# Kernel tuning notes

Measured on AMD Instinct MI355X. Metric: run time of the kernel, lower is better.

The kernel has to match this reference:

```python
import jax, jax.numpy as jnp
import numpy as np

N = 50000      # nodes
E = 800000     # edges
DIN = 500      # input feature dim
H = 128        # hidden dim
C = 40         # num classes
B = 10000      # batch_size (labeled nodes)
L = 9          # n_layers
K = 5          # topk neighbors
ALPHA = 0.5
THETA = 1.0
ETA = 0.5


def setup_inputs() -> dict:
    key = jax.random.key(0)
    ks = jax.random.split(key, 10)
    x = jax.random.normal(ks[0], (N, DIN), jnp.float32)
    edge_index = jax.random.randint(ks[1], (2, E), 0, N, dtype=jnp.int32)
    edge_weight = jax.random.uniform(ks[2], (E,), jnp.float32)
    y = jax.random.randint(ks[3], (B,), 0, C, dtype=jnp.int32)
    W1 = jax.random.normal(ks[4], (DIN, H), jnp.float32) * 0.05
    b1 = jnp.zeros((H,), jnp.float32)
    conv_w1 = jax.random.normal(ks[5], (L, H, H), jnp.float32) * 0.05
    conv_w2 = jax.random.normal(ks[6], (L, H, H), jnp.float32) * 0.05
    W2 = jax.random.normal(ks[7], (H, C), jnp.float32) * 0.05
    b2 = jnp.zeros((C,), jnp.float32)
    return dict(x=x, edge_index=edge_index, edge_weight=edge_weight, y=y,
                batch_size=B, W1=W1, b1=b1, conv_w1=conv_w1, conv_w2=conv_w2,
                W2=W2, b2=b2)


def _spmm(edge_index, edge_weight, h):
    # out[row] += w * h[col]  (sparse adj_t @ h)
    row, col = edge_index[0], edge_index[1]
    msg = h[col] * edge_weight[:, None]           # [E, H]
    return jax.ops.segment_sum(msg, row, num_segments=N)


def reference(x, edge_index, edge_weight, y, batch_size, W1, b1, conv_w1, conv_w2, W2, b2):
    # eval mode: dropout is identity, no diagonal mask in label fusion
    h = jax.nn.relu(x @ W1 + b1)                  # [N, H]
    x0 = h
    for l in range(L):
        beta = float(np.log(THETA / (l + 1) + 1.0))
        p = _spmm(edge_index, edge_weight, h) * (1.0 - ALPHA)   # propagated, scaled
        xr = ALPHA * x0                                          # initial residual
        out = ((1.0 - beta) * p + beta * (p @ conv_w1[l])
               + (1.0 - beta) * xr + beta * (xr @ conv_w2[l]))
        h = jax.nn.relu(h + out)
    emb = h[:batch_size]                          # [B, H]
    logits = h @ W2 + b2
    p_lc = jax.nn.log_softmax(logits[:batch_size], axis=1)       # [B, C]
    # kNN label fusion: cosine similarity, topk, exp-weighted one-hot sum
    an = emb / jnp.clip(jnp.linalg.norm(emb, axis=1, keepdims=True), 1e-8)
    sim = an @ an.T                               # [B, B]
    vals, idx = jax.lax.top_k(sim, K)             # [B, K]
    w = jnp.exp(jax.lax.stop_gradient(vals))      # topk computed under no_grad
    onehot = jax.nn.one_hot(y, C, dtype=jnp.float32)             # [B, C]
    fused = jnp.einsum('bk,bkc->bc', w, onehot[idx])             # [B, C]
    p_sim = jax.nn.log_softmax(fused, axis=1)
    final = ETA * p_lc + (1.0 - ETA) * p_sim
    return final, emb
```

## Files before the change

kernel.cpp:

```cpp
#include <hip/hip_runtime.h>
#include <hip/hip_bf16.h>
#include <math.h>

#define Nn  50000
#define NR  50048
#define En  800000
#define DIN 500
#define Hd  128
#define Cc  40
#define Bb  10000
#define Ll  9
#define KT  5

typedef short bf16x8 __attribute__((ext_vector_type(8)));
typedef unsigned short u16x8 __attribute__((ext_vector_type(8)));
typedef float f32x4 __attribute__((ext_vector_type(4)));

__device__ inline float bf2f(unsigned short u) {
  union { unsigned int i; float f; } c; c.i = (unsigned int)u << 16; return c.f;
}
__device__ inline unsigned short f2bf(float f) {
  __hip_bfloat16 b = __float2bfloat16(f);
  return *(unsigned short*)&b;
}

__global__ __launch_bounds__(256) void k_pack_w1(const float* __restrict__ W1,
                                                 unsigned short* __restrict__ W1p) {
  const int id = blockIdx.x * 256 + threadIdx.x;
  if (id >= 65536) return;
  const int j = id & 7, col = (id >> 3) & 127, qk = id >> 10;
  const int k = (qk >> 2) * 32 + (qk & 3) * 8 + j;
  W1p[id] = f2bf((k < DIN) ? W1[(size_t)k * Hd + col] : 0.f);
}

__global__ __launch_bounds__(256) void k_pack_wc(const float* __restrict__ cw1,
    const float* __restrict__ cw2, unsigned short* __restrict__ Wcp) {
  const int id = blockIdx.x * 256 + threadIdx.x;
  if (id >= 294912) return;
  const int j = id & 7, col = (id >> 3) & 127, qk = (id >> 10) & 31, l = id >> 15;
  const int k = (qk >> 2) * 32 + (qk & 3) * 8 + j;
  float v;
  if (k < 128) v = cw1[((size_t)l * 128 + k) * 128 + col];
  else         v = 0.5f * cw2[((size_t)l * 128 + (k - 128)) * 128 + col];
  Wcp[id] = f2bf(v);
}

__global__ __launch_bounds__(256) void k_in(const float* __restrict__ x,
    const unsigned short* __restrict__ W1p, const float* __restrict__ b1,
    unsigned short* __restrict__ hb, unsigned short* __restrict__ x0b) {
  const int tid = threadIdx.x;
  const int wv = tid >> 6, lane = tid & 63;
  const int lrow = lane & 15, quad = lane >> 4;
  const int row0 = blockIdx.x * 64;
  const int ar = row0 + wv * 16 + lrow;
  f32x4 acc[8];
#pragma unroll
  for (int t = 0; t < 8; ++t) acc[t] = (f32x4){0.f, 0.f, 0.f, 0.f};

  for (int kk = 0; kk < 16; ++kk) {
    const int kbase = kk * 32 + quad * 8;
    float av[8];
    if (ar < Nn) {
      if (kk < 15) {
        const float4 p0 = *(const float4*)(x + (size_t)ar * DIN + kbase);
        const float4 p1 = *(const float4*)(x + (size_t)ar * DIN + kbase + 4);
        av[0] = p0.x; av[1] = p0.y; av[2] = p0.z; av[3] = p0.w;
        av[4] = p1.x; av[5] = p1.y; av[6] = p1.z; av[7] = p1.w;
      } else {
#pragma unroll
        for (int j = 0; j < 8; ++j)
          av[j] = (kbase + j < DIN) ? x[(size_t)ar * DIN + kbase + j] : 0.f;
      }
    } else {
#pragma unroll
      for (int j = 0; j < 8; ++j) av[j] = 0.f;
    }
    bf16x8 af;
#pragma unroll
    for (int j = 0; j < 8; ++j) af[j] = (short)f2bf(av[j]);
#pragma unroll
    for (int nt = 0; nt < 8; ++nt) {
      const bf16x8 bf = *(const bf16x8*)(W1p + ((size_t)(kk * 4 + quad) * 128 + nt * 16 + lrow) * 8);
      acc[nt] = __builtin_amdgcn_mfma_f32_16x16x32_bf16(af, bf, acc[nt], 0, 0, 0);
    }
  }

  __shared__ float sacc[64 * 132];
#pragma unroll
  for (int nt = 0; nt < 8; ++nt)
#pragma unroll
    for (int i = 0; i < 4; ++i)
      sacc[(wv * 16 + quad * 4 + i) * 132 + nt * 16 + lrow] = acc[nt][i];
  __syncthreads();

  const int row = tid >> 2, cs = (tid & 3) * 32;
  const int gr = row0 + row;
  if (gr < Nn) {
#pragma unroll
    for (int g = 0; g < 4; ++g) {
      const int c0 = cs + g * 8;
      float v[8];
#pragma unroll
      for (int j = 0; j < 8; ++j)
        v[j] = fmaxf(sacc[row * 132 + c0 + j] + b1[c0 + j], 0.f);
      u16x8 ob;
#pragma unroll
      for (int j = 0; j < 8; ++j) ob[j] = f2bf(v[j]);
      *(u16x8*)(hb + (size_t)gr * Hd + c0) = ob;
      *(u16x8*)(x0b + (size_t)gr * Hd + c0) = ob;
    }
  }
}

__global__ void k_hist(const int* __restrict__ rows, int* __restrict__ counts) {
  int e = blockIdx.x * 256 + threadIdx.x;
  if (e < En) atomicAdd(&counts[rows[e]], 1);
}

__global__ __launch_bounds__(256) void k_scan2(const int* __restrict__ counts,
                                               int* __restrict__ rptr) {
  __shared__ int sdata[256];
  const int b = blockIdx.x, tid = threadIdx.x;
  const int npre = b << 8;
  int s0 = 0, s1 = 0, s2 = 0, s3 = 0;
  int i = tid;
  for (; i + 768 < npre; i += 1024) {
    s0 += counts[i]; s1 += counts[i + 256]; s2 += counts[i + 512]; s3 += counts[i + 768];
  }
  for (; i < npre; i += 256) s0 += counts[i];
  sdata[tid] = s0 + s1 + s2 + s3;
  __syncthreads();
  for (int off = 128; off > 0; off >>= 1) {
    if (tid < off) sdata[tid] += sdata[tid + off];
    __syncthreads();
  }
  const int base = sdata[0];
  __syncthreads();
  const int gi = npre + tid;
  int v = (gi < Nn) ? counts[gi] : 0;
  sdata[tid] = v;
  __syncthreads();
  for (int off = 1; off < 256; off <<= 1) {
    int t = (tid >= off) ? sdata[tid - off] : 0;
    __syncthreads();
    sdata[tid] += t;
    __syncthreads();
  }
  if (gi < Nn) rptr[gi + 1] = base + sdata[tid];
  if (b == 0 && tid == 0) rptr[0] = 0;
}

__global__ void k_scatter(const int* __restrict__ rows, const int* __restrict__ cols,
                          const float* __restrict__ w, const int* __restrict__ ptr,
                          int* __restrict__ fill, int* __restrict__ csr_col,
                          float* __restrict__ csr_w) {
  int e = blockIdx.x * 256 + threadIdx.x;
  if (e >= En) return;
  int r = rows[e];
  int pos = atomicAdd(&fill[r], 1);
  int d = ptr[r] + pos;
  csr_col[d] = cols[e];
  csr_w[d] = w[e];
}

__global__ __launch_bounds__(256) void k_spmm(const int* __restrict__ ptr,
    const int* __restrict__ csr_col, const float* __restrict__ csr_w,
    const unsigned short* __restrict__ hb, unsigned short* __restrict__ pb) {
  const int wave = (blockIdx.x * 256 + threadIdx.x) >> 6;
  const int lane = threadIdx.x & 63;
  const int g = lane >> 4;
  const int fl = lane & 15;
  if (wave >= Nn) return;
  const int s = ptr[wave], e_end = ptr[wave + 1];
  float acc[8];
#pragma unroll
  for (int j = 0; j < 8; ++j) acc[j] = 0.f;

  auto acc8 = [&](uint4 v, float w) {
    union { unsigned int i; float f; } t;
    t.i = v.x << 16;         acc[0] += w * t.f;
    t.i = v.x & 0xFFFF0000u; acc[1] += w * t.f;
    t.i = v.y << 16;         acc[2] += w * t.f;
    t.i = v.y & 0xFFFF0000u; acc[3] += w * t.f;
    t.i = v.z << 16;         acc[4] += w * t.f;
    t.i = v.z & 0xFFFF0000u; acc[5] += w * t.f;
    t.i = v.w << 16;         acc[6] += w * t.f;
    t.i = v.w & 0xFFFF0000u; acc[7] += w * t.f;
  };

  int e = s + g;
  for (; e + 12 < e_end; e += 16) {
    const int c0 = csr_col[e];
    const int c1 = csr_col[e + 4];
    const int c2 = csr_col[e + 8];
    const int c3 = csr_col[e + 12];
    const float w0 = csr_w[e];
    const float w1 = csr_w[e + 4];
    const float w2 = csr_w[e + 8];
    const float w3 = csr_w[e + 12];
    const uint4 v0 = *(const uint4*)(hb + (size_t)c0 * Hd + fl * 8);
    const uint4 v1 = *(const uint4*)(hb + (size_t)c1 * Hd + fl * 8);
    const uint4 v2 = *(const uint4*)(hb + (size_t)c2 * Hd + fl * 8);
    const uint4 v3 = *(const uint4*)(hb + (size_t)c3 * Hd + fl * 8);
    acc8(v0, w0); acc8(v1, w1); acc8(v2, w2); acc8(v3, w3);
  }
  for (; e + 4 < e_end; e += 8) {
    const int c0 = csr_col[e];
    const int c1 = csr_col[e + 4];
    const float w0 = csr_w[e];
    const float w1 = csr_w[e + 4];
    const uint4 v0 = *(const uint4*)(hb + (size_t)c0 * Hd + fl * 8);
    const uint4 v1 = *(const uint4*)(hb + (size_t)c1 * Hd + fl * 8);
    acc8(v0, w0); acc8(v1, w1);
  }
  if (e < e_end) {
    const int c = csr_col[e];
    const float w = csr_w[e];
    const uint4 v = *(const uint4*)(hb + (size_t)c * Hd + fl * 8);
    acc8(v, w);
  }
#pragma unroll
  for (int j = 0; j < 8; ++j) acc[j] += __shfl_xor(acc[j], 16);
#pragma unroll
  for (int j = 0; j < 8; ++j) acc[j] += __shfl_xor(acc[j], 32);
  if (g == 0) {
    uint4 o;
    o.x = (unsigned int)f2bf(0.5f * acc[0]) | ((unsigned int)f2bf(0.5f * acc[1]) << 16);
    o.y = (unsigned int)f2bf(0.5f * acc[2]) | ((unsigned int)f2bf(0.5f * acc[3]) << 16);
    o.z = (unsigned int)f2bf(0.5f * acc[4]) | ((unsigned int)f2bf(0.5f * acc[5]) << 16);
    o.w = (unsigned int)f2bf(0.5f * acc[6]) | ((unsigned int)f2bf(0.5f * acc[7]) << 16);
    *(uint4*)(pb + (size_t)wave * Hd + fl * 8) = o;
  }
}

__global__ __launch_bounds__(256) void k_layer(const unsigned short* __restrict__ pb,
    const unsigned short* __restrict__ x0b, const unsigned short* __restrict__ Wcp,
    unsigned short* __restrict__ hb, float beta) {
  const int tid = threadIdx.x;
  const int wv = tid >> 6, lane = tid & 63;
  const int lrow = lane & 15, quad = lane >> 4;
  const int row0 = blockIdx.x * 64;
  const int ar = row0 + wv * 16 + lrow;
  f32x4 acc[8];
#pragma unroll
  for (int t = 0; t < 8; ++t) acc[t] = (f32x4){0.f, 0.f, 0.f, 0.f};

#pragma unroll
  for (int kk = 0; kk < 8; ++kk) {
    const unsigned short* src = (kk < 4) ? pb : x0b;
    const int ko = (kk & 3) * 32 + quad * 8;
    const bf16x8 af = *(const bf16x8*)(src + (size_t)ar * Hd + ko);
#pragma unroll
    for (int nt = 0; nt < 8; ++nt) {
      const bf16x8 bf = *(const bf16x8*)(Wcp + ((size_t)(kk * 4 + quad) * 128 + nt * 16 + lrow) * 8);
      acc[nt] = __builtin_amdgcn_mfma_f32_16x16x32_bf16(af, bf, acc[nt], 0, 0, 0);
    }
  }

  __shared__ float sacc[64 * 132];
#pragma unroll
  for (int nt = 0; nt < 8; ++nt)
#pragma unroll
    for (int i = 0; i < 4; ++i)
      sacc[(wv * 16 + quad * 4 + i) * 132 + nt * 16 + lrow] = acc[nt][i];
  __syncthreads();

  const int row = tid >> 2, cs = (tid & 3) * 32;
  const int gr = row0 + row;
  if (gr < Nn) {
    const float om = 1.f - beta;
#pragma unroll
    for (int g = 0; g < 4; ++g) {
      const int c0 = cs + g * 8;
      const u16x8 pv = *(const u16x8*)(pb + (size_t)gr * Hd + c0);
      const u16x8 xv = *(const u16x8*)(x0b + (size_t)gr * Hd + c0);
      const u16x8 hv = *(const u16x8*)(hb + (size_t)gr * Hd + c0);
      float nv[8];
#pragma unroll
      for (int j = 0; j < 8; ++j) {
        const float gemm = sacc[row * 132 + c0 + j];
        const float pj = bf2f(pv[j]);
        const float xj = bf2f(xv[j]);
        const float outv = om * (pj + 0.5f * xj) + beta * gemm;
        nv[j] = fmaxf(bf2f(hv[j]) + outv, 0.f);
      }
      u16x8 ob;
#pragma unroll
      for (int j = 0; j < 8; ++j) ob[j] = f2bf(nv[j]);
      *(u16x8*)(hb + (size_t)gr * Hd + c0) = ob;
    }
  }
}

__global__ __launch_bounds__(256) void k_head(const unsigned short* __restrict__ hb,
    const float* __restrict__ W2, const float* __restrict__ b2,
    unsigned short* __restrict__ anb, float* __restrict__ p_lc,
    float* __restrict__ out_emb) {
  const int wid = (blockIdx.x * 256 + threadIdx.x) >> 6;
  const int lane = threadIdx.x & 63;
  if (wid >= Bb) return;
  const unsigned short* hr = hb + (size_t)wid * Hd;
  const float v0 = bf2f(hr[lane]), v1 = bf2f(hr[lane + 64]);
  out_emb[wid * Hd + lane] = v0;
  out_emb[wid * Hd + lane + 64] = v1;
  float ss = v0 * v0 + v1 * v1;
#pragma unroll
  for (int off = 32; off > 0; off >>= 1) ss += __shfl_xor(ss, off);
  const float inv = 1.f / fmaxf(sqrtf(ss), 1e-8f);
  anb[wid * Hd + lane] = f2bf(v0 * inv);
  anb[wid * Hd + lane + 64] = f2bf(v1 * inv);
  float l = 0.f;
  if (lane < Cc) {
    for (int k = 0; k < Hd; ++k) l += bf2f(hr[k]) * W2[k * Cc + lane];
    l += b2[lane];
  }
  float lm = (lane < Cc) ? l : -3.0e38f;
#pragma unroll
  for (int off = 32; off > 0; off >>= 1) lm = fmaxf(lm, __shfl_xor(lm, off));
  float ex = (lane < Cc) ? expf(l - lm) : 0.f;
#pragma unroll
  for (int off = 32; off > 0; off >>= 1) ex += __shfl_xor(ex, off);
  const float lse = logf(ex);
  if (lane < Cc) p_lc[wid * Cc + lane] = l - lm - lse;
}

#define CH_N  8
#define CH_SZ 1250
#define SB_LD 136
__global__ __launch_bounds__(256) void k_simtopk(const unsigned short* __restrict__ anb,
    float* __restrict__ cval, int* __restrict__ cidx) {
  __shared__ __align__(16) char smem[40960];
  unsigned short* sb = (unsigned short*)smem;
  const int rt = blockIdx.x / CH_N;
  const int chunk = blockIdx.x % CH_N;
  const int row0 = rt * 64;
  const int cbeg = chunk * CH_SZ;
  const int cend = cbeg + CH_SZ;
  const int tid = threadIdx.x;
  const int wv = tid >> 6;
  const int lane = tid & 63;
  const int lrow = lane & 15;
  const int quad = lane >> 4;

  union Frag { uint4 u4; bf16x8 v; };
  bf16x8 afr[4];
  const int ar = row0 + wv * 16 + lrow;
#pragma unroll
  for (int kq = 0; kq < 4; ++kq) {
    Frag f;
    f.u4 = make_uint4(0u, 0u, 0u, 0u);
    if (ar < Bb) f.u4 = *(const uint4*)(anb + (size_t)ar * Hd + kq * 32 + quad * 8);
    afr[kq] = f.v;
  }

  float bv[4][KT];
  int bi[4][KT];
#pragma unroll
  for (int r = 0; r < 4; ++r)
#pragma unroll
    for (int t = 0; t < KT; ++t) { bv[r][t] = -3.0e38f; bi[r][t] = 0x7fffffff; }
  float minthr = -3.0e38f;

  const int ntile = (CH_SZ + 63) / 64;
  for (int t = 0; t < ntile; ++t) {
    const int c0 = cbeg + t * 64;
    __syncthreads();
    for (int i = tid; i < 1024; i += 256) {
      const int r = i >> 4, ch = i & 15;
      const int gc = c0 + r;
      uint4 v = make_uint4(0u, 0u, 0u, 0u);
      if (gc < cend) v = *(const uint4*)(anb + (size_t)gc * Hd + ch * 8);
      *(uint4*)&sb[r * SB_LD + ch * 8] = v;
    }
    __syncthreads();
#pragma unroll
    for (int sub = 0; sub < 4; ++sub) {
      f32x4 acc = {0.f, 0.f, 0.f, 0.f};
      const int scol = sub * 16 + lrow;
#pragma unroll
      for (int kq = 0; kq < 4; ++kq) {
        bf16x8 bfr = *(const bf16x8*)&sb[scol * SB_LD + kq * 32 + quad * 8];
        acc = __builtin_amdgcn_mfma_f32_16x16x32_bf16(afr[kq], bfr, acc, 0, 0, 0);
      }
      const int gc = c0 + scol;
      const bool ok = gc < cend;
      float vv[4];
#pragma unroll
      for (int i = 0; i < 4; ++i) vv[i] = ok ? acc[i] : -3.0e38f;
      const float mx = fmaxf(fmaxf(vv[0], vv[1]), fmaxf(vv[2], vv[3]));
      if (mx > minthr) {
#pragma unroll
        for (int i = 0; i < 4; ++i) {
          const float v = vv[i];
          if (v > bv[i][KT - 1]) {
            float tv = v; int ti = gc;
#pragma unroll
            for (int s = 0; s < KT; ++s) {
              if (tv > bv[i][s]) {
                float ov = bv[i][s]; int oi = bi[i][s];
                bv[i][s] = tv; bi[i][s] = ti; tv = ov; ti = oi;
              }
            }
          }
        }
        minthr = fminf(fminf(bv[0][KT - 1], bv[1][KT - 1]),
                       fminf(bv[2][KT - 1], bv[3][KT - 1]));
      }
    }
  }

  __syncthreads();
  float* mv = (float*)smem;
  int* mi = (int*)(smem + 20480);
#pragma unroll
  for (int i = 0; i < 4; ++i) {
    const int row = wv * 16 + quad * 4 + i;
#pragma unroll
    for (int t = 0; t < KT; ++t) {
      mv[row * 80 + lrow * KT + t] = bv[i][t];
      mi[row * 80 + lrow * KT + t] = bi[i][t];
    }
  }
  __syncthreads();
  if (tid < 64) {
    const int gr = row0 + tid;
    if (gr < Bb) {
      float tv5[KT]; int ti5[KT];
#pragma unroll
      for (int t = 0; t < KT; ++t) { tv5[t] = -3.0e38f; ti5[t] = 0x7fffffff; }
      for (int m = 0; m < 80; ++m) {
        float v = mv[tid * 80 + m]; int id = mi[tid * 80 + m];
        if (v > tv5[KT - 1] || (v == tv5[KT - 1] && id < ti5[KT - 1])) {
#pragma unroll
          for (int s = 0; s < KT; ++s) {
            if (v > tv5[s] || (v == tv5[s] && id < ti5[s])) {
              float ov = tv5[s]; int oi = ti5[s];
              tv5[s] = v; ti5[s] = id; v = ov; id = oi;
            }
          }
        }
      }
#pragma unroll
      for (int t = 0; t < KT; ++t) {
        cval[gr * (CH_N * KT) + chunk * KT + t] = tv5[t];
        cidx[gr * (CH_N * KT) + chunk * KT + t] = ti5[t];
      }
    }
  }
}

__global__ __launch_bounds__(256) void k_final(const float* __restrict__ cval,
    const int* __restrict__ cidx, const int* __restrict__ y,
    const float* __restrict__ p_lc, float* __restrict__ out_final) {
  const int b = blockIdx.x * 256 + threadIdx.x;
  if (b >= Bb) return;
  float tv5[KT]; int ti5[KT];
#pragma unroll
  for (int t = 0; t < KT; ++t) { tv5[t] = -3.0e38f; ti5[t] = 0x7fffffff; }
#pragma unroll
  for (int m = 0; m < CH_N * KT; ++m) {
    float v = cval[b * (CH_N * KT) + m]; int id = cidx[b * (CH_N * KT) + m];
    if (v > tv5[KT - 1] || (v == tv5[KT - 1] && id < ti5[KT - 1])) {
#pragma unroll
      for (int t = 0; t < KT; ++t) {
        if (v > tv5[t] || (v == tv5[t] && id < ti5[t])) {
          float ov = tv5[t]; int oi = ti5[t];
          tv5[t] = v; ti5[t] = id; v = ov; id = oi;
        }
      }
    }
  }
  float w[KT]; int cls[KT];
#pragma unroll
  for (int t = 0; t < KT; ++t) { w[t] = expf(tv5[t]); cls[t] = y[ti5[t]]; }
  float m = -3.0e38f;
  for (int c = 0; c < Cc; ++c) {
    float f = 0.f;
#pragma unroll
    for (int t = 0; t < KT; ++t) f += (cls[t] == c) ? w[t] : 0.f;
    m = fmaxf(m, f);
  }
  float s = 0.f;
  for (int c = 0; c < Cc; ++c) {
    float f = 0.f;
#pragma unroll
    for (int t = 0; t < KT; ++t) f += (cls[t] == c) ? w[t] : 0.f;
    s += expf(f - m);
  }
  const float lse = logf(s);
  for (int c = 0; c < Cc; ++c) {
    float f = 0.f;
#pragma unroll
    for (int t = 0; t < KT; ++t) f += (cls[t] == c) ? w[t] : 0.f;
    out_final[b * Cc + c] = 0.5f * p_lc[b * Cc + c] + 0.5f * (f - m - lse);
  }
}

extern "C" void kernel_launch(void* const* d_in, const int* in_sizes, int n_in,
                              void* d_out, int out_size, void* d_ws, size_t ws_size,
                              hipStream_t stream) {
  const float* x  = (const float*)d_in[0];
  const int* erow = (const int*)d_in[1];
  const int* ecol = erow + En;
  const float* ew = (const float*)d_in[2];
  const int* y    = (const int*)d_in[3];
  const float* W1 = (const float*)d_in[5];
  const float* b1 = (const float*)d_in[6];
  const float* cw1 = (const float*)d_in[7];
  const float* cw2 = (const float*)d_in[8];
  const float* W2 = (const float*)d_in[9];
  const float* b2 = (const float*)d_in[10];
  float* out = (float*)d_out;

  float* ws = (float*)d_ws;
  size_t off = 0;
  float* plc = ws + off; off += (size_t)Bb * Cc;
  float* cval = ws + off; off += (size_t)Bb * (CH_N * KT);
  int* cidx  = (int*)(ws + off); off += (size_t)Bb * (CH_N * KT);
  int* counts = (int*)(ws + off); off += Nn;
  int* fill   = (int*)(ws + off); off += Nn;
  int* rptr   = (int*)(ws + off); off += Nn + 4;
  int* ccol   = (int*)(ws + off); off += En;
  float* cwt  = ws + off; off += En;
  unsigned short* anb = (unsigned short*)(ws + off); off += (size_t)Bb * Hd / 2;
  unsigned short* hb  = (unsigned short*)(ws + off); off += (size_t)NR * Hd / 2;
  unsigned short* x0b = (unsigned short*)(ws + off); off += (size_t)NR * Hd / 2;
  unsigned short* pb  = (unsigned short*)(ws + off); off += (size_t)NR * Hd / 2;
  unsigned short* W1p = (unsigned short*)(ws + off); off += 65536 / 2;
  unsigned short* Wcp = (unsigned short*)(ws + off); off += 294912 / 2;

  k_pack_w1<<<256, 256, 0, stream>>>(W1, W1p);
  k_pack_wc<<<1152, 256, 0, stream>>>(cw1, cw2, Wcp);
  k_in<<<NR / 64, 256, 0, stream>>>(x, W1p, b1, hb, x0b);
  hipMemsetAsync(counts, 0, (size_t)2 * Nn * sizeof(int), stream);
  k_hist<<<(En + 255) / 256, 256, 0, stream>>>(erow, counts);
  k_scan2<<<(Nn + 255) / 256, 256, 0, stream>>>(counts, rptr);
  k_scatter<<<(En + 255) / 256, 256, 0, stream>>>(erow, ecol, ew, rptr, fill, ccol, cwt);
  for (int l = 0; l < Ll; ++l) {
    const float beta = logf(1.0f / (float)(l + 1) + 1.0f);
    k_spmm<<<(Nn * 64 + 255) / 256, 256, 0, stream>>>(rptr, ccol, cwt, hb, pb);
    k_layer<<<NR / 64, 256, 0, stream>>>(pb, x0b, Wcp + (size_t)l * 32768, hb, beta);
  }
  k_head<<<(Bb * 64) / 256, 256, 0, stream>>>(hb, W2, b2, anb, plc, out + (size_t)Bb * Cc);
  k_simtopk<<<((Bb + 63) / 64) * CH_N, 256, 0, stream>>>(anb, cval, cidx);
  k_final<<<(Bb + 255) / 256, 256, 0, stream>>>(cval, cidx, y, plc, out);
}
```

Baseline: 1.012 ms.

## Interleave CSR col/weight pairs, double topk chunks, merge topk via shuffles

The CSR column and weight arrays become one interleaved int2 array, so each edge in the SpMM is fetched with a single 8-byte load instead of two separate loads. The similarity top-k kernel now splits columns into 16 chunks instead of 8 to launch more blocks. Its shared-memory per-row merge is replaced by a butterfly of wave shuffles that merges the per-lane top-5 lists in registers. This frees shared memory, but the final kernel now has twice as many candidates to merge per row and its merge loop is no longer unrolled.

```diff
diff --git a/kernel.cpp b/kernel.cpp
--- a/kernel.cpp
+++ b/kernel.cpp
@@ -152,19 +152,18 @@
 
 __global__ void k_scatter(const int* __restrict__ rows, const int* __restrict__ cols,
                           const float* __restrict__ w, const int* __restrict__ ptr,
-                          int* __restrict__ fill, int* __restrict__ csr_col,
-                          float* __restrict__ csr_w) {
+                          int* __restrict__ fill, int2* __restrict__ cpair) {
   int e = blockIdx.x * 256 + threadIdx.x;
   if (e >= En) return;
   int r = rows[e];
   int pos = atomicAdd(&fill[r], 1);
   int d = ptr[r] + pos;
-  csr_col[d] = cols[e];
-  csr_w[d] = w[e];
+  int2 pr; pr.x = cols[e]; pr.y = __float_as_int(w[e]);
+  cpair[d] = pr;
 }
 
 __global__ __launch_bounds__(256) void k_spmm(const int* __restrict__ ptr,
-    const int* __restrict__ csr_col, const float* __restrict__ csr_w,
+    const int2* __restrict__ cpair,
     const unsigned short* __restrict__ hb, unsigned short* __restrict__ pb) {
   const int wave = (blockIdx.x * 256 + threadIdx.x) >> 6;
   const int lane = threadIdx.x & 63;
@@ -190,34 +189,28 @@
 
   int e = s + g;
   for (; e + 12 < e_end; e += 16) {
-    const int c0 = csr_col[e];
-    const int c1 = csr_col[e + 4];
-    const int c2 = csr_col[e + 8];
-    const int c3 = csr_col[e + 12];
-    const float w0 = csr_w[e];
-    const float w1 = csr_w[e + 4];
-    const float w2 = csr_w[e + 8];
-    const float w3 = csr_w[e + 12];
-    const uint4 v0 = *(const uint4*)(hb + (size_t)c0 * Hd + fl * 8);
-    const uint4 v1 = *(const uint4*)(hb + (size_t)c1 * Hd + fl * 8);
-    const uint4 v2 = *(const uint4*)(hb + (size_t)c2 * Hd + fl * 8);
-    const uint4 v3 = *(const uint4*)(hb + (size_t)c3 * Hd + fl * 8);
-    acc8(v0, w0); acc8(v1, w1); acc8(v2, w2); acc8(v3, w3);
+    const int2 p0 = cpair[e];
+    const int2 p1 = cpair[e + 4];
+    const int2 p2 = cpair[e + 8];
+    const int2 p3 = cpair[e + 12];
+    const uint4 v0 = *(const uint4*)(hb + (size_t)p0.x * Hd + fl * 8);
+    const uint4 v1 = *(const uint4*)(hb + (size_t)p1.x * Hd + fl * 8);
+    const uint4 v2 = *(const uint4*)(hb + (size_t)p2.x * Hd + fl * 8);
+    const uint4 v3 = *(const uint4*)(hb + (size_t)p3.x * Hd + fl * 8);
+    acc8(v0, __int_as_float(p0.y)); acc8(v1, __int_as_float(p1.y));
+    acc8(v2, __int_as_float(p2.y)); acc8(v3, __int_as_float(p3.y));
   }
   for (; e + 4 < e_end; e += 8) {
-    const int c0 = csr_col[e];
-    const int c1 = csr_col[e + 4];
-    const float w0 = csr_w[e];
-    const float w1 = csr_w[e + 4];
-    const uint4 v0 = *(const uint4*)(hb + (size_t)c0 * Hd + fl * 8);
-    const uint4 v1 = *(const uint4*)(hb + (size_t)c1 * Hd + fl * 8);
-    acc8(v0, w0); acc8(v1, w1);
+    const int2 p0 = cpair[e];
+    const int2 p1 = cpair[e + 4];
+    const uint4 v0 = *(const uint4*)(hb + (size_t)p0.x * Hd + fl * 8);
+    const uint4 v1 = *(const uint4*)(hb + (size_t)p1.x * Hd + fl * 8);
+    acc8(v0, __int_as_float(p0.y)); acc8(v1, __int_as_float(p1.y));
   }
   if (e < e_end) {
-    const int c = csr_col[e];
-    const float w = csr_w[e];
-    const uint4 v = *(const uint4*)(hb + (size_t)c * Hd + fl * 8);
-    acc8(v, w);
+    const int2 p0 = cpair[e];
+    const uint4 v = *(const uint4*)(hb + (size_t)p0.x * Hd + fl * 8);
+    acc8(v, __int_as_float(p0.y));
   }
 #pragma unroll
   for (int j = 0; j < 8; ++j) acc[j] += __shfl_xor(acc[j], 16);
@@ -324,13 +317,12 @@
   if (lane < Cc) p_lc[wid * Cc + lane] = l - lm - lse;
 }
 
-#define CH_N  8
-#define CH_SZ 1250
+#define CH_N  16
+#define CH_SZ 625
 #define SB_LD 136
 __global__ __launch_bounds__(256) void k_simtopk(const unsigned short* __restrict__ anb,
     float* __restrict__ cval, int* __restrict__ cidx) {
-  __shared__ __align__(16) char smem[40960];
-  unsigned short* sb = (unsigned short*)smem;
+  __shared__ __align__(16) unsigned short sb[64 * SB_LD];
   const int rt = blockIdx.x / CH_N;
   const int chunk = blockIdx.x % CH_N;
   const int row0 = rt * 64;
@@ -409,41 +401,43 @@
     }
   }
 
-  __syncthreads();
-  float* mv = (float*)smem;
-  int* mi = (int*)(smem + 20480);
-#pragma unroll
-  for (int i = 0; i < 4; ++i) {
-    const int row = wv * 16 + quad * 4 + i;
-#pragma unroll
-    for (int t = 0; t < KT; ++t) {
-      mv[row * 80 + lrow * KT + t] = bv[i][t];
-      mi[row * 80 + lrow * KT + t] = bi[i][t];
-    }
-  }
-  __syncthreads();
-  if (tid < 64) {
-    const int gr = row0 + tid;
-    if (gr < Bb) {
-      float tv5[KT]; int ti5[KT];
-#pragma unroll
-      for (int t = 0; t < KT; ++t) { tv5[t] = -3.0e38f; ti5[t] = 0x7fffffff; }
-      for (int m = 0; m < 80; ++m) {
-        float v = mv[tid * 80 + m]; int id = mi[tid * 80 + m];
-        if (v > tv5[KT - 1] || (v == tv5[KT - 1] && id < ti5[KT - 1])) {
+#pragma unroll
+  for (int off = 1; off < 16; off <<= 1) {
+#pragma unroll
+    for (int i = 0; i < 4; ++i) {
+      float ov[KT]; int oi[KT];
+#pragma unroll
+      for (int t = 0; t < KT; ++t) {
+        ov[t] = __shfl_xor(bv[i][t], off);
+        oi[t] = __shfl_xor(bi[i][t], off);
+      }
+#pragma unroll
+      for (int t = 0; t < KT; ++t) {
+        float v = ov[t]; int id = oi[t];
+        if (v > bv[i][KT - 1] || (v == bv[i][KT - 1] && id < bi[i][KT - 1])) {
 #pragma unroll
           for (int s = 0; s < KT; ++s) {
-            if (v > tv5[s] || (v == tv5[s] && id < ti5[s])) {
-              float ov = tv5[s]; int oi = ti5[s];
-              tv5[s] = v; ti5[s] = id; v = ov; id = oi;
+            const bool take = (v > bv[i][s]) || (v == bv[i][s] && id < bi[i][s]);
+            if (take) {
+              float tv = bv[i][s]; int ti = bi[i][s];
+              bv[i][s] = v; bi[i][s] = id; v = tv; id = ti;
             }
           }
         }
       }
-#pragma unroll
-      for (int t = 0; t < KT; ++t) {
-        cval[gr * (CH_N * KT) + chunk * KT + t] = tv5[t];
-        cidx[gr * (CH_N * KT) + chunk * KT + t] = ti5[t];
+    }
+  }
+
+  if (lrow == 0) {
+#pragma unroll
+    for (int i = 0; i < 4; ++i) {
+      const int gr = row0 + wv * 16 + quad * 4 + i;
+      if (gr < Bb) {
+#pragma unroll
+        for (int t = 0; t < KT; ++t) {
+          cval[(size_t)gr * (CH_N * KT) + chunk * KT + t] = bv[i][t];
+          cidx[(size_t)gr * (CH_N * KT) + chunk * KT + t] = bi[i][t];
+        }
       }
     }
   }
@@ -457,9 +451,8 @@
   float tv5[KT]; int ti5[KT];
 #pragma unroll
   for (int t = 0; t < KT; ++t) { tv5[t] = -3.0e38f; ti5[t] = 0x7fffffff; }
-#pragma unroll
   for (int m = 0; m < CH_N * KT; ++m) {
-    float v = cval[b * (CH_N * KT) + m]; int id = cidx[b * (CH_N * KT) + m];
+    float v = cval[(size_t)b * (CH_N * KT) + m]; int id = cidx[(size_t)b * (CH_N * KT) + m];
     if (v > tv5[KT - 1] || (v == tv5[KT - 1] && id < ti5[KT - 1])) {
 #pragma unroll
       for (int t = 0; t < KT; ++t) {
@@ -520,8 +513,7 @@
   int* counts = (int*)(ws + off); off += Nn;
   int* fill   = (int*)(ws + off); off += Nn;
   int* rptr   = (int*)(ws + off); off += Nn + 4;
-  int* ccol   = (int*)(ws + off); off += En;
-  float* cwt  = ws + off; off += En;
+  int2* cpair = (int2*)(ws + off); off += (size_t)2 * En;
   unsigned short* anb = (unsigned short*)(ws + off); off += (size_t)Bb * Hd / 2;
   unsigned short* hb  = (unsigned short*)(ws + off); off += (size_t)NR * Hd / 2;
   unsigned short* x0b = (unsigned short*)(ws + off); off += (size_t)NR * Hd / 2;
@@ -535,10 +527,10 @@
   hipMemsetAsync(counts, 0, (size_t)2 * Nn * sizeof(int), stream);
   k_hist<<<(En + 255) / 256, 256, 0, stream>>>(erow, counts);
   k_scan2<<<(Nn + 255) / 256, 256, 0, stream>>>(counts, rptr);
-  k_scatter<<<(En + 255) / 256, 256, 0, stream>>>(erow, ecol, ew, rptr, fill, ccol, cwt);
+  k_scatter<<<(En + 255) / 256, 256, 0, stream>>>(erow, ecol, ew, rptr, fill, cpair);
   for (int l = 0; l < Ll; ++l) {
     const float beta = logf(1.0f / (float)(l + 1) + 1.0f);
-    k_spmm<<<(Nn * 64 + 255) / 256, 256, 0, stream>>>(rptr, ccol, cwt, hb, pb);
+    k_spmm<<<(Nn * 64 + 255) / 256, 256, 0, stream>>>(rptr, cpair, hb, pb);
     k_layer<<<NR / 64, 256, 0, stream>>>(pb, x0b, Wcp + (size_t)l * 32768, hb, beta);
   }
   k_head<<<(Bb * 64) / 256, 256, 0, stream>>>(hb, W2, b2, anb, plc, out + (size_t)Bb * Cc);
```

Measured after the change: 1.035 ms. 1.02x slower.
